# Performance work log

Hardware: AMD Instinct MI355X
Metric: run time of the kernel (lower is better)

## Reference

```python
import jax, jax.numpy as jnp
import numpy as np

B, S, D, H = 2, 2048, 1024, 16
HD = D // H  # head_dim = 64

def setup_inputs() -> dict:
    key = jax.random.key(0)
    ks = jax.random.split(key, 10)
    s = 1.0 / np.sqrt(D)
    return {
        "hidden_states": jax.random.normal(ks[0], (B, S, D), jnp.float32),
        "attention_mask": jnp.ones((B, S), jnp.float32),
        "q_w": jax.random.uniform(ks[1], (D, D), jnp.float32, -s, s),
        "q_b": jax.random.uniform(ks[2], (D,), jnp.float32, -s, s),
        "k_w": jax.random.uniform(ks[3], (D, D), jnp.float32, -s, s),
        "k_b": jax.random.uniform(ks[4], (D,), jnp.float32, -s, s),
        "v_w": jax.random.uniform(ks[5], (D, D), jnp.float32, -s, s),
        "v_b": jax.random.uniform(ks[6], (D,), jnp.float32, -s, s),
        "o_w": jax.random.uniform(ks[7], (D, D), jnp.float32, -s, s),
        "o_b": jax.random.uniform(ks[8], (D,), jnp.float32, -s, s),
    }

def reference(hidden_states, attention_mask, q_w, q_b, k_w, k_b, v_w, v_b, o_w, o_b):
    scale = HD ** -0.5
    # projections; torch Linear: x @ W^T + b. Here weights stored as (D, D) used directly.
    q = hidden_states @ q_w + q_b  # [B,S,D]
    k = hidden_states @ k_w + k_b
    v = hidden_states @ v_w + v_b
    # split heads -> [B,H,S,HD]
    q = q.reshape(B, S, H, HD).transpose(0, 2, 1, 3)
    k = k.reshape(B, S, H, HD).transpose(0, 2, 1, 3)
    v = v.reshape(B, S, H, HD).transpose(0, 2, 1, 3)
    scores = jnp.einsum('bhqd,bhkd->bhqk', q, k) * scale  # [B,H,S,S]
    # additive mask from 2D [B,S] mask (1=keep, 0=mask)
    scores = scores + (1.0 - attention_mask)[:, None, None, :] * -10000.0
    attn = jax.nn.softmax(scores, axis=-1)
    ctx = jnp.einsum('bhqk,bhkd->bhqd', attn, v)  # [B,H,S,HD]
    ctx = ctx.transpose(0, 2, 1, 3).reshape(B, S, D)
    return ctx @ o_w + o_b
```

## Files before the change

### kernel.cpp

```cpp
#include <hip/hip_runtime.h>
#include <hip/hip_bf16.h>

#define B_ 2
#define S_ 2048
#define D_ 1024
#define H_ 16
#define HD_ 64

#define QSCALE 0.18033688f
#define MLOG2E 14426.950408f

typedef __attribute__((ext_vector_type(8))) short bf16x8;
typedef __attribute__((ext_vector_type(4))) short short4v;
typedef __attribute__((ext_vector_type(4))) float floatx4;

static __device__ __forceinline__ float bf2f(short u) {
  union { float f; unsigned int i; } c;
  c.i = ((unsigned int)(unsigned short)u) << 16;
  return c.f;
}
static __device__ __forceinline__ short f2bf(float f) {
  union { float f; unsigned int i; } c; c.f = f;
  unsigned int r = c.i + 0x7FFFu + ((c.i >> 16) & 1u);
  return (short)(r >> 16);
}
static __device__ __forceinline__ short f2bf_fast(float f) {
  union { float f; unsigned int i; } c; c.f = f;
  return (short)((c.i + 0x8000u) >> 16);
}

static __device__ __forceinline__ void gld_lds16(const void* g, void* l) {
  __builtin_amdgcn_global_load_lds(
      (const __attribute__((address_space(1))) unsigned int*)g,
      (__attribute__((address_space(3))) unsigned int*)l, 16, 0, 0);
}

__global__ __launch_bounds__(256)
void cvt_hs(const float4* __restrict__ in, short4v* __restrict__ out) {
  const int i = blockIdx.x * 256 + threadIdx.x;
  const float4 v = in[i];
  short4v o;
  o[0] = f2bf(v.x); o[1] = f2bf(v.y); o[2] = f2bf(v.z); o[3] = f2bf(v.w);
  out[i] = o;
}

__global__ __launch_bounds__(256)
void transpose4(const float* __restrict__ w0, const float* __restrict__ w1,
                const float* __restrict__ w2, const float* __restrict__ w3,
                short* __restrict__ out) {
  __shared__ short t[64][65];
  const int z = blockIdx.z;
  const float* src = z == 0 ? w0 : z == 1 ? w1 : z == 2 ? w2 : w3;
  short* dst = out + (size_t)z * D_ * D_;
  const int tx = threadIdx.x & 63, ty = threadIdx.x >> 6;
  const int r0 = blockIdx.y * 64, c0 = blockIdx.x * 64;
  for (int r = ty; r < 64; r += 4)
    t[r][tx] = f2bf(src[(size_t)(r0 + r) * D_ + c0 + tx]);
  __syncthreads();
  for (int r = ty; r < 64; r += 4)
    dst[(size_t)(c0 + r) * D_ + r0 + tx] = t[tx][r];
}

__global__ __launch_bounds__(256, 2)
void gemm_qkv(const short* __restrict__ X, const short* __restrict__ WT,
              const float* __restrict__ qb, const float* __restrict__ kb,
              const float* __restrict__ vb,
              short* __restrict__ Qo, short* __restrict__ Ko,
              short* __restrict__ Vt) {
  __shared__ __align__(16) short As[128 * 32];
  __shared__ __align__(16) short Bs[128 * 32];
  const int tid = threadIdx.x;
  const int wave = tid >> 6, lane = tid & 63;
  const int col = lane & 15, quad = lane >> 4;
  const int m0 = blockIdx.x * 128;
  const int nt = blockIdx.y;
  const int widx = nt >> 3;
  const int n1 = (nt & 7) * 128;
  const short* Bsrc = WT + (size_t)widx * D_ * D_ + (size_t)n1 * D_;
  const int b = m0 >> 11;

  const int srow = tid >> 2;
  const int skcol = (tid & 3) * 8;
  const short* ga = X + (size_t)(m0 + srow) * D_ + skcol;
  const short* gb = Bsrc + (size_t)srow * D_ + skcol;
  short* la = As + tid * 8;
  short* lb = Bs + tid * 8;

  floatx4 acc[4][4];
#pragma unroll
  for (int i = 0; i < 4; i++)
#pragma unroll
    for (int j = 0; j < 4; j++) acc[i][j] = floatx4{0.f, 0.f, 0.f, 0.f};

  if (widx < 2) {
    const int wseq = (wave >> 1) * 64;
    const int wfeat = (wave & 1) * 64;
    for (int k0 = 0; k0 < D_; k0 += 32) {
      gld_lds16(ga, la);
      gld_lds16(ga + 64 * D_, la + 2048);
      gld_lds16(gb, lb);
      gld_lds16(gb + 64 * D_, lb + 2048);
      ga += 32; gb += 32;
      __syncthreads();
      bf16x8 xf[4], wf[4];
#pragma unroll
      for (int j = 0; j < 4; j++)
        xf[j] = *(const bf16x8*)(As + (wseq + j * 16 + col) * 32 + quad * 8);
#pragma unroll
      for (int i = 0; i < 4; i++)
        wf[i] = *(const bf16x8*)(Bs + (wfeat + i * 16 + col) * 32 + quad * 8);
#pragma unroll
      for (int i = 0; i < 4; i++)
#pragma unroll
        for (int j = 0; j < 4; j++)
          acc[i][j] = __builtin_amdgcn_mfma_f32_16x16x32_bf16(wf[i], xf[j],
                                                              acc[i][j], 0, 0, 0);
      __syncthreads();
    }
    const float* bias = widx == 0 ? qb : kb;
    short* dst = widx == 0 ? Qo : Ko;
    const float scale = widx == 0 ? QSCALE : 1.0f;
#pragma unroll
    for (int i = 0; i < 4; i++) {
      const int nf = n1 + wfeat + i * 16 + quad * 4;
      const int h = nf >> 6, hd = nf & 63;
      const float4 bv = *(const float4*)(bias + nf);
#pragma unroll
      for (int j = 0; j < 4; j++) {
        const int s = (m0 + wseq + j * 16 + col) & (S_ - 1);
        short4v pk;
        pk[0] = f2bf((acc[i][j][0] + bv.x) * scale);
        pk[1] = f2bf((acc[i][j][1] + bv.y) * scale);
        pk[2] = f2bf((acc[i][j][2] + bv.z) * scale);
        pk[3] = f2bf((acc[i][j][3] + bv.w) * scale);
        *(short4v*)(dst + ((size_t)(b * H_ + h) * S_ + s) * HD_ + hd) = pk;
      }
    }
  } else {
    const int wrow = (wave & 1) * 64;
    const int wcol = (wave >> 1) * 64;
    for (int k0 = 0; k0 < D_; k0 += 32) {
      gld_lds16(ga, la);
      gld_lds16(ga + 64 * D_, la + 2048);
      gld_lds16(gb, lb);
      gld_lds16(gb + 64 * D_, lb + 2048);
      ga += 32; gb += 32;
      __syncthreads();
      bf16x8 af[4], bfr[4];
#pragma unroll
      for (int i = 0; i < 4; i++)
        af[i] = *(const bf16x8*)(As + (wrow + i * 16 + col) * 32 + quad * 8);
#pragma unroll
      for (int j = 0; j < 4; j++)
        bfr[j] = *(const bf16x8*)(Bs + (wcol + j * 16 + col) * 32 + quad * 8);
#pragma unroll
      for (int i = 0; i < 4; i++)
#pragma unroll
        for (int j = 0; j < 4; j++)
          acc[i][j] = __builtin_amdgcn_mfma_f32_16x16x32_bf16(af[i], bfr[j],
                                                              acc[i][j], 0, 0, 0);
      __syncthreads();
    }
    float bv[4];
#pragma unroll
    for (int j = 0; j < 4; j++) bv[j] = vb[n1 + wcol + j * 16 + col];
#pragma unroll
    for (int i = 0; i < 4; i++) {
      const int s = (m0 + wrow + i * 16 + quad * 4) & (S_ - 1);
#pragma unroll
      for (int j = 0; j < 4; j++) {
        const int nl = n1 + wcol + j * 16 + col;
        const int h = nl >> 6, hd = nl & 63;
        short4v pk;
#pragma unroll
        for (int r = 0; r < 4; r++) pk[r] = f2bf(acc[i][j][r] + bv[j]);
        *(short4v*)(Vt + ((size_t)(b * H_ + h) * HD_ + hd) * S_ + s) = pk;
      }
    }
  }
}

__global__ __launch_bounds__(256, 3)
void attn(const short* __restrict__ Q, const short* __restrict__ K,
          const short* __restrict__ Vt, const float* __restrict__ mask,
          short* __restrict__ ctx) {
  __shared__ __align__(16) short Ks[2][4096];
  __shared__ __align__(16) short Vs[2][4096];
  __shared__ __align__(16) short P[4][16][72];
  __shared__ float m2s[S_];
  const int tid = threadIdx.x, wave = tid >> 6, lane = tid & 63;
  const int col = lane & 15, quad = lane >> 4;
  const int qt = blockIdx.x, h = blockIdx.y, b = blockIdx.z;
  const short* Qh = Q + (size_t)(b * H_ + h) * S_ * HD_;
  const short* Kh = K + (size_t)(b * H_ + h) * S_ * HD_;
  const short* Vh = Vt + (size_t)(b * H_ + h) * HD_ * S_;
  const float* mk = mask + (size_t)b * S_;
  const int q0 = qt * 64 + wave * 16;

  const int r1 = tid >> 3, c1 = (tid & 7) ^ (r1 & 7);
  const int r2 = r1 + 32,  c2 = (tid & 7) ^ (r2 & 7);
  const int swz = quad ^ (col & 7);

  for (int i = tid; i < S_ / 4; i += 256) {
    const float4 mv = ((const float4*)mk)[i];
    float4 o;
    o.x = mv.x * MLOG2E - MLOG2E;
    o.y = mv.y * MLOG2E - MLOG2E;
    o.z = mv.z * MLOG2E - MLOG2E;
    o.w = mv.w * MLOG2E - MLOG2E;
    ((float4*)m2s)[i] = o;
  }
  gld_lds16(Kh + (size_t)r1 * HD_ + c1 * 8, &Ks[0][tid * 8]);
  gld_lds16(Kh + (size_t)r2 * HD_ + c2 * 8, &Ks[0][(tid + 256) * 8]);
  gld_lds16(Vh + (size_t)r1 * S_ + c1 * 8, &Vs[0][tid * 8]);
  gld_lds16(Vh + (size_t)r2 * S_ + c2 * 8, &Vs[0][(tid + 256) * 8]);

  const bf16x8 qf0 = *(const bf16x8*)(Qh + (size_t)(q0 + col) * HD_ + quad * 8);
  const bf16x8 qf1 = *(const bf16x8*)(Qh + (size_t)(q0 + col) * HD_ + 32 + quad * 8);

  floatx4 acc[4];
#pragma unroll
  for (int d = 0; d < 4; d++) acc[d] = floatx4{0.f, 0.f, 0.f, 0.f};
  float rs[4] = {0.f, 0.f, 0.f, 0.f};

  __syncthreads();

  for (int it = 0; it < S_ / 64; it++) {
    const int buf = it & 1;
    const int kt = it * 64;
    if (it + 1 < S_ / 64) {
      const int kn = kt + 64;
      gld_lds16(Kh + (size_t)(kn + r1) * HD_ + c1 * 8, &Ks[buf ^ 1][tid * 8]);
      gld_lds16(Kh + (size_t)(kn + r2) * HD_ + c2 * 8, &Ks[buf ^ 1][(tid + 256) * 8]);
      gld_lds16(Vh + (size_t)r1 * S_ + kn + c1 * 8, &Vs[buf ^ 1][tid * 8]);
      gld_lds16(Vh + (size_t)r2 * S_ + kn + c2 * 8, &Vs[buf ^ 1][(tid + 256) * 8]);
    }

    float m2v[4];
#pragma unroll
    for (int t = 0; t < 4; t++) m2v[t] = m2s[kt + t * 16 + col];

    float p[4][4];
#pragma unroll
    for (int t = 0; t < 4; t++) {
      const short* kp = &Ks[buf][(t * 16 + col) * 64];
      const bf16x8 kf0 = *(const bf16x8*)(kp + swz * 8);
      const bf16x8 kf1 = *(const bf16x8*)(kp + (swz ^ 4) * 8);
      floatx4 z = floatx4{0.f, 0.f, 0.f, 0.f};
      z = __builtin_amdgcn_mfma_f32_16x16x32_bf16(qf0, kf0, z, 0, 0, 0);
      z = __builtin_amdgcn_mfma_f32_16x16x32_bf16(qf1, kf1, z, 0, 0, 0);
#pragma unroll
      for (int r = 0; r < 4; r++) p[t][r] = exp2f(z[r] + m2v[t]);
    }
#pragma unroll
    for (int t = 0; t < 4; t++)
#pragma unroll
      for (int r = 0; r < 4; r++) {
        rs[r] += p[t][r];
        P[wave][quad * 4 + r][t * 16 + col] = f2bf_fast(p[t][r]);
      }

    bf16x8 pf[2];
#pragma unroll
    for (int kk = 0; kk < 2; kk++) {
      const short4v p0 = *(const short4v*)&P[wave][col][kk * 32 + quad * 8];
      const short4v p1 = *(const short4v*)&P[wave][col][kk * 32 + quad * 8 + 4];
      bf16x8 pv;
      pv[0] = p0[0]; pv[1] = p0[1]; pv[2] = p0[2]; pv[3] = p0[3];
      pv[4] = p1[0]; pv[5] = p1[1]; pv[6] = p1[2]; pv[7] = p1[3];
      pf[kk] = pv;
    }
#pragma unroll
    for (int d = 0; d < 4; d++) {
      const short* vp = &Vs[buf][(d * 16 + col) * 64];
      const bf16x8 vf0 = *(const bf16x8*)(vp + swz * 8);
      const bf16x8 vf1 = *(const bf16x8*)(vp + (swz ^ 4) * 8);
      acc[d] = __builtin_amdgcn_mfma_f32_16x16x32_bf16(pf[0], vf0, acc[d], 0, 0, 0);
      acc[d] = __builtin_amdgcn_mfma_f32_16x16x32_bf16(pf[1], vf1, acc[d], 0, 0, 0);
    }
    __syncthreads();
  }

#pragma unroll
  for (int r = 0; r < 4; r++) {
    float v = rs[r];
    v += __shfl_xor(v, 1); v += __shfl_xor(v, 2);
    v += __shfl_xor(v, 4); v += __shfl_xor(v, 8);
    rs[r] = 1.0f / (v + 1e-30f);
  }
#pragma unroll
  for (int d = 0; d < 4; d++)
#pragma unroll
    for (int r = 0; r < 4; r++)
      ctx[((size_t)b * S_ + q0 + quad * 4 + r) * D_ + h * HD_ + d * 16 + col] =
          f2bf(acc[d][r] * rs[r]);
}

__global__ __launch_bounds__(256, 2)
void gemm_out(const short* __restrict__ X, const short* __restrict__ WT,
              const float* __restrict__ ob, float* __restrict__ out) {
  __shared__ __align__(16) short As[128 * 32];
  __shared__ __align__(16) short Bs[128 * 32];
  const int tid = threadIdx.x;
  const int wave = tid >> 6, lane = tid & 63;
  const int col = lane & 15, quad = lane >> 4;
  const int m0 = blockIdx.x * 128;
  const int n0 = blockIdx.y * 128;
  const short* Bsrc = WT + (size_t)n0 * D_;
  const int wrow = (wave & 1) * 64;
  const int wcol = (wave >> 1) * 64;

  floatx4 acc[4][4];
#pragma unroll
  for (int i = 0; i < 4; i++)
#pragma unroll
    for (int j = 0; j < 4; j++) acc[i][j] = floatx4{0.f, 0.f, 0.f, 0.f};

  const int srow = tid >> 2;
  const int skcol = (tid & 3) * 8;
  const short* ga = X + (size_t)(m0 + srow) * D_ + skcol;
  const short* gb = Bsrc + (size_t)srow * D_ + skcol;
  short* la = As + tid * 8;
  short* lb = Bs + tid * 8;

  for (int k0 = 0; k0 < D_; k0 += 32) {
    gld_lds16(ga, la);
    gld_lds16(ga + 64 * D_, la + 2048);
    gld_lds16(gb, lb);
    gld_lds16(gb + 64 * D_, lb + 2048);
    ga += 32; gb += 32;
    __syncthreads();
    bf16x8 af[4], bfr[4];
#pragma unroll
    for (int i = 0; i < 4; i++)
      af[i] = *(const bf16x8*)(As + (wrow + i * 16 + col) * 32 + quad * 8);
#pragma unroll
    for (int j = 0; j < 4; j++)
      bfr[j] = *(const bf16x8*)(Bs + (wcol + j * 16 + col) * 32 + quad * 8);
#pragma unroll
    for (int i = 0; i < 4; i++)
#pragma unroll
      for (int j = 0; j < 4; j++)
        acc[i][j] = __builtin_amdgcn_mfma_f32_16x16x32_bf16(af[i], bfr[j],
                                                            acc[i][j], 0, 0, 0);
    __syncthreads();
  }

  float bv[4];
#pragma unroll
  for (int j = 0; j < 4; j++) bv[j] = ob[n0 + wcol + j * 16 + col];

#pragma unroll
  for (int i = 0; i < 4; i++) {
    const int m = m0 + wrow + i * 16 + quad * 4;
#pragma unroll
    for (int j = 0; j < 4; j++) {
      const int n = n0 + wcol + j * 16 + col;
#pragma unroll
      for (int r = 0; r < 4; r++)
        out[(size_t)(m + r) * D_ + n] = acc[i][j][r] + bv[j];
    }
  }
}

extern "C" void kernel_launch(void* const* d_in, const int* in_sizes, int n_in,
                              void* d_out, int out_size, void* d_ws, size_t ws_size,
                              hipStream_t stream) {
  (void)in_sizes; (void)n_in; (void)out_size; (void)ws_size;
  const float* hs  = (const float*)d_in[0];
  const float* msk = (const float*)d_in[1];
  const float* qw  = (const float*)d_in[2];
  const float* qb  = (const float*)d_in[3];
  const float* kw  = (const float*)d_in[4];
  const float* kb  = (const float*)d_in[5];
  const float* vw  = (const float*)d_in[6];
  const float* vb  = (const float*)d_in[7];
  const float* ow  = (const float*)d_in[8];
  const float* ob  = (const float*)d_in[9];
  float* out = (float*)d_out;
  char* ws = (char*)d_ws;

  short* Xb  = (short*)(ws);
  short* WT  = (short*)(ws + (8ull  << 20));
  short* Qp  = (short*)(ws + (16ull << 20));
  short* Kp  = (short*)(ws + (24ull << 20));
  short* Vtp = (short*)(ws + (32ull << 20));
  short* Ctx = Xb;

  cvt_hs<<<dim3(4096), 256, 0, stream>>>((const float4*)hs, (short4v*)Xb);
  transpose4<<<dim3(16, 16, 4), 256, 0, stream>>>(qw, kw, vw, ow, WT);
  gemm_qkv<<<dim3(32, 24), 256, 0, stream>>>(Xb, WT, qb, kb, vb, Qp, Kp, Vtp);
  attn<<<dim3(32, 16, 2), 256, 0, stream>>>(Qp, Kp, Vtp, msk, Ctx);
  gemm_out<<<dim3(32, 8), 256, 0, stream>>>(Ctx, WT + 3ull * D_ * D_, ob, out);
}
```

Measured before the change: 232.3 us.

## Double query rows per attention wave, MFMA row sums, fuse prep kernels

The attention kernel now gives each wave 32 query rows in two groups, so each K/V tile loaded from LDS is reused across both groups and the grid is halved. Row sums are computed with an MFMA against a ones vector instead of scalar adds and shuffles, and the operand order in the PV MFMA is swapped so the output can be written as packed short4 stores. The mask is read from global memory every iteration instead of being staged in LDS. Separately, the bf16 convert and weight transpose kernels are merged into one launch, and the launch bounds for gemm_qkv and attn are changed. Costs: more registers in attn, fewer attention blocks to fill the GPU, and extra global mask loads inside the loop.

```diff
diff --git a/kernel.cpp b/kernel.cpp
--- a/kernel.cpp
+++ b/kernel.cpp
@@ -36,32 +36,38 @@
 }
 
 __global__ __launch_bounds__(256)
-void cvt_hs(const float4* __restrict__ in, short4v* __restrict__ out) {
-  const int i = blockIdx.x * 256 + threadIdx.x;
-  const float4 v = in[i];
-  short4v o;
-  o[0] = f2bf(v.x); o[1] = f2bf(v.y); o[2] = f2bf(v.z); o[3] = f2bf(v.w);
-  out[i] = o;
-}
-
-__global__ __launch_bounds__(256)
-void transpose4(const float* __restrict__ w0, const float* __restrict__ w1,
-                const float* __restrict__ w2, const float* __restrict__ w3,
-                short* __restrict__ out) {
-  __shared__ short t[64][65];
+void prep(const float* __restrict__ w0, const float* __restrict__ w1,
+          const float* __restrict__ w2, const float* __restrict__ w3,
+          const float* __restrict__ hs, short* __restrict__ WT,
+          short* __restrict__ Xb) {
   const int z = blockIdx.z;
-  const float* src = z == 0 ? w0 : z == 1 ? w1 : z == 2 ? w2 : w3;
-  short* dst = out + (size_t)z * D_ * D_;
-  const int tx = threadIdx.x & 63, ty = threadIdx.x >> 6;
-  const int r0 = blockIdx.y * 64, c0 = blockIdx.x * 64;
-  for (int r = ty; r < 64; r += 4)
-    t[r][tx] = f2bf(src[(size_t)(r0 + r) * D_ + c0 + tx]);
-  __syncthreads();
-  for (int r = ty; r < 64; r += 4)
-    dst[(size_t)(c0 + r) * D_ + r0 + tx] = t[tx][r];
-}
-
-__global__ __launch_bounds__(256, 2)
+  if (z < 4) {
+    __shared__ short t[64][65];
+    const float* src = z == 0 ? w0 : z == 1 ? w1 : z == 2 ? w2 : w3;
+    short* dst = WT + (size_t)z * D_ * D_;
+    const int tx = threadIdx.x & 63, ty = threadIdx.x >> 6;
+    const int r0 = blockIdx.y * 64, c0 = blockIdx.x * 64;
+    for (int r = ty; r < 64; r += 4)
+      t[r][tx] = f2bf(src[(size_t)(r0 + r) * D_ + c0 + tx]);
+    __syncthreads();
+    for (int r = ty; r < 64; r += 4)
+      dst[(size_t)(c0 + r) * D_ + r0 + tx] = t[tx][r];
+  } else {
+    const int bid = blockIdx.y * 16 + blockIdx.x;
+    const float4* in4 = (const float4*)hs;
+    short4v* out4 = (short4v*)Xb;
+#pragma unroll
+    for (int i = 0; i < 16; i++) {
+      const int idx = bid * 4096 + i * 256 + threadIdx.x;
+      const float4 v = in4[idx];
+      short4v o;
+      o[0] = f2bf(v.x); o[1] = f2bf(v.y); o[2] = f2bf(v.z); o[3] = f2bf(v.w);
+      out4[idx] = o;
+    }
+  }
+}
+
+__global__ __launch_bounds__(256, 3)
 void gemm_qkv(const short* __restrict__ X, const short* __restrict__ WT,
               const float* __restrict__ qb, const float* __restrict__ kb,
               const float* __restrict__ vb,
@@ -180,14 +186,13 @@
   }
 }
 
-__global__ __launch_bounds__(256, 3)
+__global__ __launch_bounds__(256, 2)
 void attn(const short* __restrict__ Q, const short* __restrict__ K,
           const short* __restrict__ Vt, const float* __restrict__ mask,
           short* __restrict__ ctx) {
   __shared__ __align__(16) short Ks[2][4096];
   __shared__ __align__(16) short Vs[2][4096];
-  __shared__ __align__(16) short P[4][16][72];
-  __shared__ float m2s[S_];
+  __shared__ __align__(16) short P[4][2][16][68];
   const int tid = threadIdx.x, wave = tid >> 6, lane = tid & 63;
   const int col = lane & 15, quad = lane >> 4;
   const int qt = blockIdx.x, h = blockIdx.y, b = blockIdx.z;
@@ -195,33 +200,36 @@
   const short* Kh = K + (size_t)(b * H_ + h) * S_ * HD_;
   const short* Vh = Vt + (size_t)(b * H_ + h) * HD_ * S_;
   const float* mk = mask + (size_t)b * S_;
-  const int q0 = qt * 64 + wave * 16;
+  const int q0 = qt * 128 + wave * 32;
 
   const int r1 = tid >> 3, c1 = (tid & 7) ^ (r1 & 7);
   const int r2 = r1 + 32,  c2 = (tid & 7) ^ (r2 & 7);
   const int swz = quad ^ (col & 7);
 
-  for (int i = tid; i < S_ / 4; i += 256) {
-    const float4 mv = ((const float4*)mk)[i];
-    float4 o;
-    o.x = mv.x * MLOG2E - MLOG2E;
-    o.y = mv.y * MLOG2E - MLOG2E;
-    o.z = mv.z * MLOG2E - MLOG2E;
-    o.w = mv.w * MLOG2E - MLOG2E;
-    ((float4*)m2s)[i] = o;
-  }
   gld_lds16(Kh + (size_t)r1 * HD_ + c1 * 8, &Ks[0][tid * 8]);
   gld_lds16(Kh + (size_t)r2 * HD_ + c2 * 8, &Ks[0][(tid + 256) * 8]);
   gld_lds16(Vh + (size_t)r1 * S_ + c1 * 8, &Vs[0][tid * 8]);
   gld_lds16(Vh + (size_t)r2 * S_ + c2 * 8, &Vs[0][(tid + 256) * 8]);
 
-  const bf16x8 qf0 = *(const bf16x8*)(Qh + (size_t)(q0 + col) * HD_ + quad * 8);
-  const bf16x8 qf1 = *(const bf16x8*)(Qh + (size_t)(q0 + col) * HD_ + 32 + quad * 8);
-
-  floatx4 acc[4];
-#pragma unroll
-  for (int d = 0; d < 4; d++) acc[d] = floatx4{0.f, 0.f, 0.f, 0.f};
-  float rs[4] = {0.f, 0.f, 0.f, 0.f};
+  bf16x8 qf[2][2];
+#pragma unroll
+  for (int g = 0; g < 2; g++) {
+    const short* qp = Qh + (size_t)(q0 + g * 16 + col) * HD_;
+    qf[g][0] = *(const bf16x8*)(qp + quad * 8);
+    qf[g][1] = *(const bf16x8*)(qp + 32 + quad * 8);
+  }
+
+  bf16x8 ones;
+#pragma unroll
+  for (int i = 0; i < 8; i++) ones[i] = (short)0x3F80;
+
+  floatx4 acc[2][4], rsacc[2];
+#pragma unroll
+  for (int g = 0; g < 2; g++) {
+    rsacc[g] = floatx4{0.f, 0.f, 0.f, 0.f};
+#pragma unroll
+    for (int d = 0; d < 4; d++) acc[g][d] = floatx4{0.f, 0.f, 0.f, 0.f};
+  }
 
   __syncthreads();
 
@@ -238,62 +246,73 @@
 
     float m2v[4];
 #pragma unroll
-    for (int t = 0; t < 4; t++) m2v[t] = m2s[kt + t * 16 + col];
-
-    float p[4][4];
+    for (int t = 0; t < 4; t++)
+      m2v[t] = mk[kt + t * 16 + col] * MLOG2E - MLOG2E;
+
+    bf16x8 kf[4][2];
 #pragma unroll
     for (int t = 0; t < 4; t++) {
       const short* kp = &Ks[buf][(t * 16 + col) * 64];
-      const bf16x8 kf0 = *(const bf16x8*)(kp + swz * 8);
-      const bf16x8 kf1 = *(const bf16x8*)(kp + (swz ^ 4) * 8);
-      floatx4 z = floatx4{0.f, 0.f, 0.f, 0.f};
-      z = __builtin_amdgcn_mfma_f32_16x16x32_bf16(qf0, kf0, z, 0, 0, 0);
-      z = __builtin_amdgcn_mfma_f32_16x16x32_bf16(qf1, kf1, z, 0, 0, 0);
-#pragma unroll
-      for (int r = 0; r < 4; r++) p[t][r] = exp2f(z[r] + m2v[t]);
-    }
-#pragma unroll
-    for (int t = 0; t < 4; t++)
-#pragma unroll
-      for (int r = 0; r < 4; r++) {
-        rs[r] += p[t][r];
-        P[wave][quad * 4 + r][t * 16 + col] = f2bf_fast(p[t][r]);
+      kf[t][0] = *(const bf16x8*)(kp + swz * 8);
+      kf[t][1] = *(const bf16x8*)(kp + (swz ^ 4) * 8);
+    }
+
+#pragma unroll
+    for (int g = 0; g < 2; g++)
+#pragma unroll
+      for (int t = 0; t < 4; t++) {
+        floatx4 z = floatx4{0.f, 0.f, 0.f, 0.f};
+        z = __builtin_amdgcn_mfma_f32_16x16x32_bf16(qf[g][0], kf[t][0], z, 0, 0, 0);
+        z = __builtin_amdgcn_mfma_f32_16x16x32_bf16(qf[g][1], kf[t][1], z, 0, 0, 0);
+#pragma unroll
+        for (int r = 0; r < 4; r++)
+          P[wave][g][quad * 4 + r][t * 16 + col] = f2bf_fast(exp2f(z[r] + m2v[t]));
       }
 
-    bf16x8 pf[2];
-#pragma unroll
-    for (int kk = 0; kk < 2; kk++) {
-      const short4v p0 = *(const short4v*)&P[wave][col][kk * 32 + quad * 8];
-      const short4v p1 = *(const short4v*)&P[wave][col][kk * 32 + quad * 8 + 4];
-      bf16x8 pv;
-      pv[0] = p0[0]; pv[1] = p0[1]; pv[2] = p0[2]; pv[3] = p0[3];
-      pv[4] = p1[0]; pv[5] = p1[1]; pv[6] = p1[2]; pv[7] = p1[3];
-      pf[kk] = pv;
+    bf16x8 pf[2][2];
+#pragma unroll
+    for (int g = 0; g < 2; g++)
+#pragma unroll
+      for (int kk = 0; kk < 2; kk++) {
+        const short4v p0 = *(const short4v*)&P[wave][g][col][kk * 32 + quad * 8];
+        const short4v p1 = *(const short4v*)&P[wave][g][col][kk * 32 + quad * 8 + 4];
+        bf16x8 pv;
+        pv[0] = p0[0]; pv[1] = p0[1]; pv[2] = p0[2]; pv[3] = p0[3];
+        pv[4] = p1[0]; pv[5] = p1[1]; pv[6] = p1[2]; pv[7] = p1[3];
+        pf[g][kk] = pv;
+      }
+
+#pragma unroll
+    for (int g = 0; g < 2; g++) {
+      rsacc[g] = __builtin_amdgcn_mfma_f32_16x16x32_bf16(ones, pf[g][0], rsacc[g], 0, 0, 0);
+      rsacc[g] = __builtin_amdgcn_mfma_f32_16x16x32_bf16(ones, pf[g][1], rsacc[g], 0, 0, 0);
     }
 #pragma unroll
     for (int d = 0; d < 4; d++) {
       const short* vp = &Vs[buf][(d * 16 + col) * 64];
       const bf16x8 vf0 = *(const bf16x8*)(vp + swz * 8);
       const bf16x8 vf1 = *(const bf16x8*)(vp + (swz ^ 4) * 8);
-      acc[d] = __builtin_amdgcn_mfma_f32_16x16x32_bf16(pf[0], vf0, acc[d], 0, 0, 0);
-      acc[d] = __builtin_amdgcn_mfma_f32_16x16x32_bf16(pf[1], vf1, acc[d], 0, 0, 0);
+#pragma unroll
+      for (int g = 0; g < 2; g++) {
+        acc[g][d] = __builtin_amdgcn_mfma_f32_16x16x32_bf16(vf0, pf[g][0], acc[g][d], 0, 0, 0);
+        acc[g][d] = __builtin_amdgcn_mfma_f32_16x16x32_bf16(vf1, pf[g][1], acc[g][d], 0, 0, 0);
+      }
     }
     __syncthreads();
   }
 
 #pragma unroll
-  for (int r = 0; r < 4; r++) {
-    float v = rs[r];
-    v += __shfl_xor(v, 1); v += __shfl_xor(v, 2);
-    v += __shfl_xor(v, 4); v += __shfl_xor(v, 8);
-    rs[r] = 1.0f / (v + 1e-30f);
-  }
-#pragma unroll
-  for (int d = 0; d < 4; d++)
-#pragma unroll
-    for (int r = 0; r < 4; r++)
-      ctx[((size_t)b * S_ + q0 + quad * 4 + r) * D_ + h * HD_ + d * 16 + col] =
-          f2bf(acc[d][r] * rs[r]);
+  for (int g = 0; g < 2; g++) {
+    const float inv = 1.0f / (rsacc[g][0] + 1e-30f);
+    const size_t row = (size_t)b * S_ + q0 + g * 16 + col;
+#pragma unroll
+    for (int d = 0; d < 4; d++) {
+      short4v o;
+#pragma unroll
+      for (int r = 0; r < 4; r++) o[r] = f2bf(acc[g][d][r] * inv);
+      *(short4v*)(ctx + row * D_ + h * HD_ + d * 16 + quad * 4) = o;
+    }
+  }
 }
 
 __global__ __launch_bounds__(256, 2)
@@ -387,9 +406,8 @@
   short* Vtp = (short*)(ws + (32ull << 20));
   short* Ctx = Xb;
 
-  cvt_hs<<<dim3(4096), 256, 0, stream>>>((const float4*)hs, (short4v*)Xb);
-  transpose4<<<dim3(16, 16, 4), 256, 0, stream>>>(qw, kw, vw, ow, WT);
+  prep<<<dim3(16, 16, 5), 256, 0, stream>>>(qw, kw, vw, ow, hs, WT, Xb);
   gemm_qkv<<<dim3(32, 24), 256, 0, stream>>>(Xb, WT, qb, kb, vb, Qp, Kp, Vtp);
-  attn<<<dim3(32, 16, 2), 256, 0, stream>>>(Qp, Kp, Vtp, msk, Ctx);
+  attn<<<dim3(16, 16, 2), 256, 0, stream>>>(Qp, Kp, Vtp, msk, Ctx);
   gemm_out<<<dim3(32, 8), 256, 0, stream>>>(Ctx, WT + 3ull * D_ * D_, ob, out);
 }
```

New measurement: 227.5 us. 1.02x faster.
